# Optimization experiments

Hardware: AMD Instinct MI355X
Metric: run time of the kernel (lower is better)

The kernel has to match this reference:

```python
import jax, jax.numpy as jnp
import numpy as np

N_HEAD = 16

def setup_inputs() -> dict:
    key = jax.random.key(0)
    ks = jax.random.split(key, 5)
    B, T, C, H, P = 2, 2048, 1024, N_HEAD, 2048
    D = C // H
    x = jax.random.normal(ks[0], (B, T, C), dtype=jnp.float32)
    W_attn = jax.random.normal(ks[1], (C, 3 * C), dtype=jnp.float32) * 0.02
    W_proj = jax.random.normal(ks[2], (C, C), dtype=jnp.float32) * 0.02
    cache_k = jax.random.normal(ks[3], (B, H, P, D), dtype=jnp.float32)
    cache_v = jax.random.normal(ks[4], (B, H, P, D), dtype=jnp.float32)
    return {"x": x, "W_attn": W_attn, "W_proj": W_proj, "cache_k": cache_k, "cache_v": cache_v}

def reference(x, W_attn, W_proj, cache_k, cache_v):
    B, T, C = x.shape
    H = N_HEAD
    D = C // H
    P = cache_k.shape[2]
    scale = 1.0 / jnp.sqrt(jnp.float32(D))
    # QKV projection (c_attn, no bias)
    qkv = x @ W_attn                                     # [B,T,3C]
    q, k, v = jnp.split(qkv, 3, axis=-1)
    q = q.reshape(B, T, H, D).transpose(0, 2, 1, 3)      # [B,H,T,D]
    k = k.reshape(B, T, H, D).transpose(0, 2, 1, 3)
    v = v.reshape(B, T, H, D).transpose(0, 2, 1, 3)
    # pos_emb_closure modeled as identity (adapt_queries/keys/attention passthrough)
    # prefix scores against cached keys (cache retrieve_for_query)
    att_prefix = jnp.einsum('bhqd,bhpd->bhqp', q, cache_k) * scale   # [B,H,T,P]
    # current causal scores
    att = jnp.einsum('bhqd,bhkd->bhqk', q, k) * scale                # [B,H,T,T]
    causal = jnp.tril(jnp.ones((T, T), dtype=bool))
    att = jnp.where(causal[None, None], att, jnp.float32(-jnp.inf))
    # fused softmax over [prefix | current]
    att_full = jax.nn.softmax(jnp.concatenate([att_prefix, att], axis=-1), axis=-1)
    att_prefix, att = att_full[..., :P], att_full[..., P:]
    # AV merge: current values + cached prefix values
    y = jnp.einsum('bhqk,bhkd->bhqd', att, v)
    y = y + jnp.einsum('bhqp,bhpd->bhqd', att_prefix, cache_v)
    y = y.transpose(0, 2, 1, 3).reshape(B, T, C)
    return y @ W_proj
```

## Files before the change

### kernel.cpp

```cpp
#include <hip/hip_runtime.h>
#include <stdint.h>

typedef unsigned short u16;
typedef unsigned int u32;
typedef short bf16x8 __attribute__((ext_vector_type(8)));
typedef float f32x4 __attribute__((ext_vector_type(4)));
typedef u32 u32x4 __attribute__((ext_vector_type(4)));

#define DEVI static __device__ __forceinline__

#define B_ 2
#define T_ 2048
#define C_ 1024
#define H_ 16
#define D_ 64
#define P_ 2048
#define M_ (B_ * T_)
#define N1_ (3 * C_)
#define LOG2E 1.44269504088896340736f

DEVI u16 f2bf(float f) {
  union { float f; u32 u; } v; v.f = f;
  u32 r = v.u + 0x7fffu + ((v.u >> 16) & 1u);
  return (u16)(r >> 16);
}

DEVI u32 cvtpk(float lo, float hi) {
  u32 r;
  asm("v_cvt_pk_bf16_f32 %0, %1, %2" : "=v"(r) : "v"(lo), "v"(hi));
  return r;
}

DEVI void gld_lds16(const void* g, void* l) {
  __builtin_amdgcn_global_load_lds((__attribute__((address_space(1))) void*)g,
                                   (__attribute__((address_space(3))) void*)l,
                                   16, 0, 0);
}

DEVI f32x4 mfma16(bf16x8 a, bf16x8 b, f32x4 c) {
  return __builtin_amdgcn_mfma_f32_16x16x32_bf16(a, b, c, 0, 0, 0);
}

__global__ void k_cast(const float* __restrict__ src, u16* __restrict__ dst, int n) {
  int i = (blockIdx.x * 256 + threadIdx.x) * 4;
  if (i >= n) return;
  float4 v = *(const float4*)(src + i);
  ushort4 o;
  o.x = f2bf(v.x); o.y = f2bf(v.y); o.z = f2bf(v.z); o.w = f2bf(v.w);
  *(ushort4*)(dst + i) = o;
}

__global__ void k_tcast(const float* __restrict__ src, u16* __restrict__ dst,
                        int R, int C) {
  __shared__ float t[32][33];
  int c0 = blockIdx.x * 32, r0 = blockIdx.y * 32;
  int tx = threadIdx.x, ty = threadIdx.y;
  for (int i = ty; i < 32; i += 8)
    t[i][tx] = src[(size_t)(r0 + i) * C + c0 + tx];
  __syncthreads();
  for (int i = ty; i < 32; i += 8)
    dst[(size_t)(c0 + i) * R + r0 + tx] = f2bf(t[tx][i]);
}

__global__ void k_tcastv(const float* __restrict__ src, u16* __restrict__ dst) {
  __shared__ float t[32][33];
  int bh = blockIdx.z;
  int p0 = blockIdx.x * 32, d0 = blockIdx.y * 32;
  int tx = threadIdx.x, ty = threadIdx.y;
  const float* s = src + ((size_t)bh * P_ + p0) * D_ + d0;
  for (int i = ty; i < 32; i += 8)
    t[i][tx] = s[(size_t)i * D_ + tx];
  __syncthreads();
  u16* d = dst + ((size_t)bh * D_ + d0) * P_ + p0;
  for (int i = ty; i < 32; i += 8)
    d[(size_t)i * P_ + tx] = f2bf(t[tx][i]);
}

template <int MODE>
__launch_bounds__(256)
__global__ void k_gemm(const u16* __restrict__ A, const u16* __restrict__ Bt,
                       void* __restrict__ out0, void* __restrict__ out1,
                       void* __restrict__ out2, int N, int K) {
  __shared__ __align__(16) u16 lA[2][128 * 32];
  __shared__ __align__(16) u16 lB[2][128 * 32];
  const int tid = threadIdx.x, lane = tid & 63, wid = tid >> 6;
  const int wr = wid >> 1, wc = wid & 1;
  const int c = lane & 15, g = lane >> 4;
  const int nt = blockIdx.x, mt = blockIdx.y;
  const int nk = K >> 5;

  f32x4 acc[4][4] = {};

  auto stage = [&](int buf, int kt) {
    for (int r = 0; r < 2; ++r) {
      int ci = wid * 2 + r;
      int row = ci * 16 + (lane >> 2);
      int gb = ((lane & 3) * 16) ^ ((row & 3) << 4);
      gld_lds16((const char*)A + ((size_t)(mt * 128 + row) * K + kt * 32) * 2 + gb,
                &lA[buf][ci * 512]);
      gld_lds16((const char*)Bt + ((size_t)(nt * 128 + row) * K + kt * 32) * 2 + gb,
                &lB[buf][ci * 512]);
    }
  };

  stage(0, 0);
  int cur = 0;
  for (int kt = 0; kt < nk; ++kt) {
    __syncthreads();
    if (kt + 1 < nk) stage(cur ^ 1, kt + 1);
    const char* pa = (const char*)&lA[cur][0];
    const char* pb = (const char*)&lB[cur][0];
    bf16x8 af[4], bfr[4];
#pragma unroll
    for (int i = 0; i < 4; ++i) {
      int ar = wr * 64 + i * 16 + c;
      af[i] = *(const bf16x8*)(pa + ar * 64 + ((g * 16) ^ ((ar & 3) << 4)));
      int br = wc * 64 + i * 16 + c;
      bfr[i] = *(const bf16x8*)(pb + br * 64 + ((g * 16) ^ ((br & 3) << 4)));
    }
#pragma unroll
    for (int i = 0; i < 4; ++i)
#pragma unroll
      for (int j = 0; j < 4; ++j)
        acc[i][j] = mfma16(af[i], bfr[j], acc[i][j]);
    cur ^= 1;
  }

  if (MODE == 0) {
    const float qs = 0.125f * LOG2E;
#pragma unroll
    for (int i = 0; i < 4; ++i) {
      int rbase = mt * 128 + wr * 64 + i * 16 + g * 4;
#pragma unroll
      for (int j = 0; j < 4; ++j) {
        int col = nt * 128 + wc * 64 + j * 16 + c;
        int which = col >> 10, cc = col & 1023;
        int h = cc >> 6, d = cc & 63;
        if (which == 2) {
          ushort4 o;
          o.x = f2bf(acc[i][j][0]); o.y = f2bf(acc[i][j][1]);
          o.z = f2bf(acc[i][j][2]); o.w = f2bf(acc[i][j][3]);
          int b = rbase >> 11, t0 = rbase & 2047;
          *(ushort4*)&((u16*)out2)[((size_t)((b * H_ + h) * D_) + d) * T_ + t0] = o;
        } else {
          u16* dst = which == 0 ? (u16*)out0 : (u16*)out1;
          float sc = which == 0 ? qs : 1.0f;
#pragma unroll
          for (int r = 0; r < 4; ++r) {
            int m = rbase + r;
            int b = m >> 11, t = m & 2047;
            dst[((size_t)(b * H_ + h) * T_ + t) * D_ + d] = f2bf(acc[i][j][r] * sc);
          }
        }
      }
    }
  } else {
    float* O = (float*)out0;
#pragma unroll
    for (int i = 0; i < 4; ++i) {
      int rbase = mt * 128 + wr * 64 + i * 16 + g * 4;
#pragma unroll
      for (int j = 0; j < 4; ++j) {
        int col = nt * 128 + wc * 64 + j * 16 + c;
#pragma unroll
        for (int r = 0; r < 4; ++r)
          O[(size_t)(rbase + r) * N + col] = acc[i][j][r];
      }
    }
  }
}

__launch_bounds__(128, 2)
__global__ void k_attn(const u16* __restrict__ qt, const u16* __restrict__ kts,
                       const u16* __restrict__ svT, const u16* __restrict__ ckb,
                       const u16* __restrict__ cvT, u16* __restrict__ y) {
  __shared__ __align__(16) u16 lK[2][64 * 64];
  __shared__ __align__(16) u16 lV[2][64 * 64];
  const int tid = threadIdx.x, lane = tid & 63, wid = tid >> 6;
  const int c = lane & 15, g = lane >> 4;
  const int qtile = blockIdx.x, bh = blockIdx.y;
  const int qbase = qtile * 64;
  const size_t hoff = (size_t)bh * (P_ * D_);

  bf16x8 qf[2][2];
#pragma unroll
  for (int qb = 0; qb < 2; ++qb) {
    const u16* qp = qt + hoff + (size_t)(qbase + wid * 32 + qb * 16 + c) * D_;
    qf[qb][0] = *(const bf16x8*)(qp + g * 8);
    qf[qb][1] = *(const bf16x8*)(qp + 32 + g * 8);
  }

  int ofsK[4][2], ofsV[4][2];
  {
    int r0 = ((c >> 1) & 1) * 32 + (c >> 2) * 8 + (c & 1);
#pragma unroll
    for (int n = 0; n < 4; ++n) {
      int R = 2 * n + r0;
      int h = (R ^ (R >> 3)) & 7;
      ofsK[n][0] = R * 128 + ((g * 16) ^ (h * 16));
      ofsK[n][1] = R * 128 + ((64 + g * 16) ^ (h * 16));
    }
#pragma unroll
    for (int db = 0; db < 4; ++db) {
      int R = db * 16 + c;
      int h = (R ^ (R >> 3)) & 7;
      ofsV[db][0] = R * 128 + ((g * 16) ^ (h * 16));
      ofsV[db][1] = R * 128 + ((64 + g * 16) ^ (h * 16));
    }
  }

  float m_[2] = {-3.0e38f, -3.0e38f}, l_[2] = {0.f, 0.f};
  f32x4 acc[2][4] = {};

  const int nPre = P_ / 64;
  const int ntl = nPre + qtile + 1;

  auto stage = [&](int buf, int t) {
    const u16* kb = (t < nPre) ? ckb + hoff + (size_t)t * 64 * D_
                               : kts + hoff + (size_t)(t - nPre) * 64 * D_;
#pragma unroll
    for (int q = 0; q < 4; ++q) {
      int chunk = q * 128 + wid * 64 + lane;
      int R = chunk >> 3, s = chunk & 7;
      int h = (R ^ (R >> 3)) & 7;
      gld_lds16((const char*)kb + R * 128 + ((s * 16) ^ (h * 16)),
                (char*)&lK[buf][0] + (q * 128 + wid * 64) * 16);
    }
    const u16* vb = (t < nPre) ? cvT + hoff : svT + hoff;
    int key0 = ((t < nPre) ? t : (t - nPre)) * 64;
#pragma unroll
    for (int q = 0; q < 4; ++q) {
      int chunk = q * 128 + wid * 64 + lane;
      int R = chunk >> 3, s = chunk & 7;
      int h = (R ^ (R >> 3)) & 7;
      gld_lds16((const char*)(vb + (size_t)R * T_ + key0) + ((s * 16) ^ (h * 16)),
                (char*)&lV[buf][0] + (q * 128 + wid * 64) * 16);
    }
  };

  stage(0, 0);
  int cur = 0;
  for (int t = 0; t < ntl; ++t) {
    __syncthreads();
    if (t + 1 < ntl) stage(cur ^ 1, t + 1);

    const char* pk = (const char*)&lK[cur][0];
    const char* pv = (const char*)&lV[cur][0];
    bf16x8 kf[4][2], vf[4][2];
#pragma unroll
    for (int n = 0; n < 4; ++n) {
      kf[n][0] = *(const bf16x8*)(pk + ofsK[n][0]);
      kf[n][1] = *(const bf16x8*)(pk + ofsK[n][1]);
    }
#pragma unroll
    for (int db = 0; db < 4; ++db) {
      vf[db][0] = *(const bf16x8*)(pv + ofsV[db][0]);
      vf[db][1] = *(const bf16x8*)(pv + ofsV[db][1]);
    }
    const bool lastT = (t == ntl - 1);

#pragma unroll
    for (int qb = 0; qb < 2; ++qb) {
      f32x4 s4[4];
#pragma unroll
      for (int n = 0; n < 4; ++n) {
        f32x4 z = {};
        z = mfma16(kf[n][0], qf[qb][0], z);
        z = mfma16(kf[n][1], qf[qb][1], z);
        s4[n] = z;
      }
      if (lastT) {
        int qloc = wid * 32 + qb * 16 + c;
#pragma unroll
        for (int n = 0; n < 4; ++n)
#pragma unroll
          for (int r = 0; r < 4; ++r) {
            int key = 2 * n + (r >> 1) * 32 + 8 * g + (r & 1);
            if (key > qloc) s4[n][r] = -3.0e38f;
          }
      }
      float mx = fmaxf(fmaxf(fmaxf(s4[0][0], s4[0][1]), fmaxf(s4[0][2], s4[0][3])),
                       fmaxf(fmaxf(s4[1][0], s4[1][1]), fmaxf(s4[1][2], s4[1][3])));
      mx = fmaxf(mx, fmaxf(fmaxf(fmaxf(s4[2][0], s4[2][1]), fmaxf(s4[2][2], s4[2][3])),
                           fmaxf(fmaxf(s4[3][0], s4[3][1]), fmaxf(s4[3][2], s4[3][3]))));
      mx = fmaxf(mx, __shfl_xor(mx, 16));
      mx = fmaxf(mx, __shfl_xor(mx, 32));
      float mn = fmaxf(m_[qb], mx);
      float alpha = exp2f(m_[qb] - mn);
      m_[qb] = mn;
      float p[4][4];
      float sum = 0.f;
#pragma unroll
      for (int n = 0; n < 4; ++n)
#pragma unroll
        for (int r = 0; r < 4; ++r) {
          p[n][r] = exp2f(s4[n][r] - mn);
          sum += p[n][r];
        }
      sum += __shfl_xor(sum, 16);
      sum += __shfl_xor(sum, 32);
      l_[qb] = l_[qb] * alpha + sum;
#pragma unroll
      for (int db = 0; db < 4; ++db) acc[qb][db] *= alpha;
      union { u32x4 w; bf16x8 v; } pa0, pa1;
#pragma unroll
      for (int jw = 0; jw < 4; ++jw) {
        pa0.w[jw] = cvtpk(p[jw][0], p[jw][1]);
        pa1.w[jw] = cvtpk(p[jw][2], p[jw][3]);
      }
#pragma unroll
      for (int db = 0; db < 4; ++db) {
        acc[qb][db] = mfma16(vf[db][0], pa0.v, acc[qb][db]);
        acc[qb][db] = mfma16(vf[db][1], pa1.v, acc[qb][db]);
      }
    }
    cur ^= 1;
  }

  const int b = bh >> 4, h = bh & 15;
#pragma unroll
  for (int qb = 0; qb < 2; ++qb) {
    float inv = 1.0f / l_[qb];
    int trow = qbase + wid * 32 + qb * 16 + c;
    size_t rowoff = ((size_t)(b * T_ + trow)) * C_ + h * D_;
#pragma unroll
    for (int db = 0; db < 4; ++db) {
      ushort4 o;
      o.x = f2bf(acc[qb][db][0] * inv);
      o.y = f2bf(acc[qb][db][1] * inv);
      o.z = f2bf(acc[qb][db][2] * inv);
      o.w = f2bf(acc[qb][db][3] * inv);
      *(ushort4*)&y[rowoff + db * 16 + 4 * g] = o;
    }
  }
}

extern "C" void kernel_launch(void* const* d_in, const int* in_sizes, int n_in,
                              void* d_out, int out_size, void* d_ws, size_t ws_size,
                              hipStream_t stream) {
  const float* x  = (const float*)d_in[0];
  const float* Wa = (const float*)d_in[1];
  const float* Wp = (const float*)d_in[2];
  const float* ck = (const float*)d_in[3];
  const float* cv = (const float*)d_in[4];
  float* out = (float*)d_out;
  char* ws = (char*)d_ws;

  u16* xb  = (u16*)(ws + (size_t)0);
  u16* waT = (u16*)(ws + (size_t)8  * 1024 * 1024);
  u16* wpT = (u16*)(ws + (size_t)14 * 1024 * 1024);
  u16* qtb = (u16*)(ws + (size_t)16 * 1024 * 1024);
  u16* ktb = (u16*)(ws + (size_t)24 * 1024 * 1024);
  u16* svT = (u16*)(ws + (size_t)32 * 1024 * 1024);
  u16* ckb = (u16*)(ws + (size_t)40 * 1024 * 1024);
  u16* cvT = (u16*)(ws + (size_t)48 * 1024 * 1024);
  u16* yb  = (u16*)(ws + (size_t)56 * 1024 * 1024);

  k_cast<<<4096, 256, 0, stream>>>(x, xb, M_ * C_);
  k_tcast<<<dim3(N1_ / 32, C_ / 32), dim3(32, 8), 0, stream>>>(Wa, waT, C_, N1_);
  k_tcast<<<dim3(C_ / 32, C_ / 32), dim3(32, 8), 0, stream>>>(Wp, wpT, C_, C_);
  k_cast<<<4096, 256, 0, stream>>>(ck, ckb, B_ * H_ * P_ * D_);
  k_tcastv<<<dim3(P_ / 32, D_ / 32, B_ * H_), dim3(32, 8), 0, stream>>>(cv, cvT);

  k_gemm<0><<<dim3(N1_ / 128, M_ / 128), 256, 0, stream>>>(xb, waT, qtb, ktb, svT, N1_, C_);
  k_attn<<<dim3(T_ / 64, B_ * H_), 128, 0, stream>>>(qtb, ktb, svT, ckb, cvT, yb);
  k_gemm<1><<<dim3(C_ / 128, M_ / 128), 256, 0, stream>>>(yb, wpT, out, nullptr, nullptr, C_, C_);
}
```

Baseline: 339.6 us.

## Load attention K/V directly to registers and pair causal q-tiles per block

```diff
diff --git a/kernel.cpp b/kernel.cpp
--- a/kernel.cpp
+++ b/kernel.cpp
@@ -170,95 +170,55 @@
   }
 }
 
-__launch_bounds__(128, 2)
+__launch_bounds__(256, 2)
 __global__ void k_attn(const u16* __restrict__ qt, const u16* __restrict__ kts,
                        const u16* __restrict__ svT, const u16* __restrict__ ckb,
                        const u16* __restrict__ cvT, u16* __restrict__ y) {
-  __shared__ __align__(16) u16 lK[2][64 * 64];
-  __shared__ __align__(16) u16 lV[2][64 * 64];
   const int tid = threadIdx.x, lane = tid & 63, wid = tid >> 6;
   const int c = lane & 15, g = lane >> 4;
-  const int qtile = blockIdx.x, bh = blockIdx.y;
-  const int qbase = qtile * 64;
+  const int pair = blockIdx.x, bh = blockIdx.y;
+  const int qtile = (((wid >> 1) ^ bh) & 1) ? (31 - pair) : pair;
+  const int qrow0 = qtile * 64 + (wid & 1) * 32;
+  const int ntl = 33 + qtile;
   const size_t hoff = (size_t)bh * (P_ * D_);
 
   bf16x8 qf[2][2];
 #pragma unroll
   for (int qb = 0; qb < 2; ++qb) {
-    const u16* qp = qt + hoff + (size_t)(qbase + wid * 32 + qb * 16 + c) * D_;
+    const u16* qp = qt + hoff + (size_t)(qrow0 + qb * 16 + c) * D_;
     qf[qb][0] = *(const bf16x8*)(qp + g * 8);
     qf[qb][1] = *(const bf16x8*)(qp + 32 + g * 8);
   }
 
-  int ofsK[4][2], ofsV[4][2];
-  {
-    int r0 = ((c >> 1) & 1) * 32 + (c >> 2) * 8 + (c & 1);
-#pragma unroll
-    for (int n = 0; n < 4; ++n) {
-      int R = 2 * n + r0;
-      int h = (R ^ (R >> 3)) & 7;
-      ofsK[n][0] = R * 128 + ((g * 16) ^ (h * 16));
-      ofsK[n][1] = R * 128 + ((64 + g * 16) ^ (h * 16));
-    }
-#pragma unroll
-    for (int db = 0; db < 4; ++db) {
-      int R = db * 16 + c;
-      int h = (R ^ (R >> 3)) & 7;
-      ofsV[db][0] = R * 128 + ((g * 16) ^ (h * 16));
-      ofsV[db][1] = R * 128 + ((64 + g * 16) ^ (h * 16));
-    }
-  }
+  const int r0 = ((c >> 1) & 1) * 32 + (c >> 2) * 8 + (c & 1);
+
+  const char* kpre  = (const char*)(ckb + hoff) + r0 * 128 + g * 16;
+  const char* kself = (const char*)(kts + hoff) + r0 * 128 + g * 16;
+  const u16* vpre  = cvT + hoff + (size_t)c * T_ + g * 8;
+  const u16* vself = svT + hoff + (size_t)c * T_ + g * 8;
 
   float m_[2] = {-3.0e38f, -3.0e38f}, l_[2] = {0.f, 0.f};
   f32x4 acc[2][4] = {};
 
-  const int nPre = P_ / 64;
-  const int ntl = nPre + qtile + 1;
-
-  auto stage = [&](int buf, int t) {
-    const u16* kb = (t < nPre) ? ckb + hoff + (size_t)t * 64 * D_
-                               : kts + hoff + (size_t)(t - nPre) * 64 * D_;
-#pragma unroll
-    for (int q = 0; q < 4; ++q) {
-      int chunk = q * 128 + wid * 64 + lane;
-      int R = chunk >> 3, s = chunk & 7;
-      int h = (R ^ (R >> 3)) & 7;
-      gld_lds16((const char*)kb + R * 128 + ((s * 16) ^ (h * 16)),
-                (char*)&lK[buf][0] + (q * 128 + wid * 64) * 16);
-    }
-    const u16* vb = (t < nPre) ? cvT + hoff : svT + hoff;
-    int key0 = ((t < nPre) ? t : (t - nPre)) * 64;
-#pragma unroll
-    for (int q = 0; q < 4; ++q) {
-      int chunk = q * 128 + wid * 64 + lane;
-      int R = chunk >> 3, s = chunk & 7;
-      int h = (R ^ (R >> 3)) & 7;
-      gld_lds16((const char*)(vb + (size_t)R * T_ + key0) + ((s * 16) ^ (h * 16)),
-                (char*)&lV[buf][0] + (q * 128 + wid * 64) * 16);
+  auto loadK = [&](bf16x8 (&kf)[4][2], int t) {
+    const char* kb = (t < 32) ? kpre + (size_t)t * 8192
+                              : kself + (size_t)(t - 32) * 8192;
+#pragma unroll
+    for (int n = 0; n < 4; ++n) {
+      kf[n][0] = *(const bf16x8*)(kb + n * 256);
+      kf[n][1] = *(const bf16x8*)(kb + n * 256 + 64);
     }
   };
-
-  stage(0, 0);
-  int cur = 0;
-  for (int t = 0; t < ntl; ++t) {
-    __syncthreads();
-    if (t + 1 < ntl) stage(cur ^ 1, t + 1);
-
-    const char* pk = (const char*)&lK[cur][0];
-    const char* pv = (const char*)&lV[cur][0];
-    bf16x8 kf[4][2], vf[4][2];
-#pragma unroll
-    for (int n = 0; n < 4; ++n) {
-      kf[n][0] = *(const bf16x8*)(pk + ofsK[n][0]);
-      kf[n][1] = *(const bf16x8*)(pk + ofsK[n][1]);
-    }
+  auto loadV = [&](bf16x8 (&vf)[4][2], int t) {
+    const u16* vb = (t < 32) ? vpre + t * 64 : vself + (t - 32) * 64;
 #pragma unroll
     for (int db = 0; db < 4; ++db) {
-      vf[db][0] = *(const bf16x8*)(pv + ofsV[db][0]);
-      vf[db][1] = *(const bf16x8*)(pv + ofsV[db][1]);
-    }
-    const bool lastT = (t == ntl - 1);
-
+      vf[db][0] = *(const bf16x8*)(vb + db * (16 * T_));
+      vf[db][1] = *(const bf16x8*)(vb + db * (16 * T_) + 32);
+    }
+  };
+
+  auto compute = [&](bf16x8 (&kf)[4][2], bf16x8 (&vf)[4][2], bool lastT) {
 #pragma unroll
     for (int qb = 0; qb < 2; ++qb) {
       f32x4 s4[4];
@@ -270,7 +230,7 @@
         s4[n] = z;
       }
       if (lastT) {
-        int qloc = wid * 32 + qb * 16 + c;
+        int qloc = (wid & 1) * 32 + qb * 16 + c;
 #pragma unroll
         for (int n = 0; n < 4; ++n)
 #pragma unroll
@@ -314,14 +274,27 @@
         acc[qb][db] = mfma16(vf[db][1], pa1.v, acc[qb][db]);
       }
     }
-    cur ^= 1;
+  };
+
+  bf16x8 kfA[4][2], kfB[4][2], vf[4][2];
+  loadK(kfA, 0);
+  int t = 0;
+  for (;;) {
+    loadV(vf, t);
+    if (t + 1 < ntl) loadK(kfB, t + 1);
+    compute(kfA, vf, t == ntl - 1);
+    if (++t >= ntl) break;
+    loadV(vf, t);
+    if (t + 1 < ntl) loadK(kfA, t + 1);
+    compute(kfB, vf, t == ntl - 1);
+    if (++t >= ntl) break;
   }
 
   const int b = bh >> 4, h = bh & 15;
 #pragma unroll
   for (int qb = 0; qb < 2; ++qb) {
     float inv = 1.0f / l_[qb];
-    int trow = qbase + wid * 32 + qb * 16 + c;
+    int trow = qrow0 + qb * 16 + c;
     size_t rowoff = ((size_t)(b * T_ + trow)) * C_ + h * D_;
 #pragma unroll
     for (int db = 0; db < 4; ++db) {
@@ -363,6 +336,6 @@
   k_tcastv<<<dim3(P_ / 32, D_ / 32, B_ * H_), dim3(32, 8), 0, stream>>>(cv, cvT);
 
   k_gemm<0><<<dim3(N1_ / 128, M_ / 128), 256, 0, stream>>>(xb, waT, qtb, ktb, svT, N1_, C_);
-  k_attn<<<dim3(T_ / 64, B_ * H_), 128, 0, stream>>>(qtb, ktb, svT, ckb, cvT, yb);
+  k_attn<<<dim3(16, B_ * H_), 256, 0, stream>>>(qtb, ktb, svT, ckb, cvT, yb);
   k_gemm<1><<<dim3(C_ / 128, M_ / 128), 256, 0, stream>>>(yb, wpT, out, nullptr, nullptr, C_, C_);
 }
```

Measured after the change: 363.4 us. 1.07x slower.
